# Kernel tuning notes

Measured on AMD Instinct MI355X. Metric: run time of the kernel, lower is better.

## Reference

```python
import jax, jax.numpy as jnp
import numpy as np
import math

B, C, D, H, W = 1, 64, 16, 16, 16
HEADS = 4
HD = C // HEADS  # head_dim = 16


def conv3d(x, w, b, pad):
    # x: [B,C,D,H,W], w: [O,I,kd,kh,kw], pad: (pd,ph,pw)
    y = jax.lax.conv_general_dilated(
        x, w, window_strides=(1, 1, 1),
        padding=[(p, p) for p in pad],
        dimension_numbers=('NCDHW', 'OIDHW', 'NCDHW'))
    return y + b[None, :, None, None, None]


def setup_inputs() -> dict:
    key = jax.random.key(0)
    ks = jax.random.split(key, 10)
    s = 0.02
    return {
        'x': jax.random.normal(ks[0], (B, C, D, H, W), jnp.float32),
        'gamma': jax.random.normal(ks[1], (1,), jnp.float32),
        'w_sp': jax.random.normal(ks[2], (C, C, 1, 3, 3), jnp.float32) * s,
        'b_sp': jax.random.normal(ks[3], (C,), jnp.float32) * s,
        'w_spec': jax.random.normal(ks[4], (C, C, 3, 1, 1), jnp.float32) * s,
        'b_spec': jax.random.normal(ks[5], (C,), jnp.float32) * s,
        'w_qkv': jax.random.normal(ks[6], (3 * C, C, 1, 1, 1), jnp.float32) * s,
        'b_qkv': jax.random.normal(ks[7], (3 * C,), jnp.float32) * s,
        'w_proj': jax.random.normal(ks[8], (C, C, 1, 1, 1), jnp.float32) * s,
        'b_proj': jax.random.normal(ks[9], (C,), jnp.float32) * s,
    }


def _decay_exponent(dtype):
    # Faithful to the torch permute quirk (requires H == W):
    # exponent[i,j,k,m,n,o] = |i-m| + |j-k| + |n-o|
    dd = jnp.abs(jnp.arange(D)[:, None] - jnp.arange(D)[None, :]).astype(dtype)  # [D,D]
    hh = jnp.abs(jnp.arange(H)[:, None] - jnp.arange(H)[None, :]).astype(dtype)  # [H,H]
    ww = jnp.abs(jnp.arange(W)[:, None] - jnp.arange(W)[None, :]).astype(dtype)  # [W,W]
    return (dd[:, None, None, :, None, None]      # i (axis0), m (axis3)
            + hh[None, :, :, None, None, None]    # j (axis1), k (axis2)
            + ww[None, None, None, None, :, :])   # n (axis4), o (axis5)


def _forward(x, gamma, w_sp, b_sp, w_spec, b_spec, w_qkv, b_qkv, w_proj, b_proj):
    x = conv3d(x, w_sp, b_sp, (0, 1, 1))
    x = conv3d(x, w_spec, b_spec, (1, 0, 0))
    qkv = conv3d(x, w_qkv, b_qkv, (0, 0, 0))
    q, k, v = jnp.split(qkv, 3, axis=1)
    rs = lambda t: t.reshape(B, HEADS, HD, D, H, W)
    q, k, v = rs(q), rs(k), rs(v)

    g = jax.nn.sigmoid(gamma[0])
    decay = g ** _decay_exponent(x.dtype)  # [D,H,W,D,W,W] (H==W)

    # attn[b,h,i,j,k,m,n,o]: (i,j,k)=query D,H,W ; (m,n,o)=key D,H,W
    attn = jnp.einsum('bhdijk,bhdmno->bhijkmno', q, k) / math.sqrt(HD)
    attn = jax.nn.softmax(attn * decay, axis=-1)  # softmax over key-W axis o only
    out = jnp.einsum('bhijkmno,bhdmno->bhdijk', attn, v)
    out = out.reshape(B, C, D, H, W)
    return conv3d(out, w_proj, b_proj, (0, 0, 0))


def reference(x, gamma, w_sp, b_sp, w_spec, b_spec, w_qkv, b_qkv, w_proj, b_proj):
    return _forward(x, gamma, w_sp, b_sp, w_spec, b_spec, w_qkv, b_qkv, w_proj, b_proj)
```

## Files before the change

### kernel.cpp

```cpp
#include <hip/hip_runtime.h>
#include <math.h>

#define CN   262144
#define BTP 196
#define PTP 68

typedef __attribute__((ext_vector_type(8))) short short8;
typedef __attribute__((ext_vector_type(4))) short short4v;
typedef __attribute__((ext_vector_type(4))) float float4v;

static __device__ __forceinline__ unsigned short f2bf(float f) {
    union { float f; unsigned u; } v; v.f = f;
    unsigned r = (v.u + 0x7FFFu + ((v.u >> 16) & 1u)) >> 16;
    return (unsigned short)r;
}

__global__ __launch_bounds__(512, 4) void conv_sp_wfuse_kernel(
        const float* __restrict__ x, const float* __restrict__ w,
        const float* __restrict__ b, float* __restrict__ y,
        const float* __restrict__ w_spec, const float* __restrict__ b_spec,
        const float* __restrict__ w_qkv, const float* __restrict__ b_qkv,
        unsigned short* __restrict__ wfb, float* __restrict__ bfv) {
    if (blockIdx.x >= 1024) {
        int idx = (blockIdx.x - 1024) * 512 + threadIdx.x;
        int oc = idx / 192;
        int r  = idx % 192;
        float s = 0.f;
        #pragma unroll 8
        for (int ci = 0; ci < 64; ++ci)
            s += w_qkv[oc * 64 + ci] * w_spec[ci * 192 + r];
        if (oc < 64) s *= 0.25f;
        wfb[oc * 192 + r] = f2bf(s);
        if (idx < 192) {
            float t = b_qkv[idx];
            for (int ci = 0; ci < 64; ++ci) t += w_qkv[idx * 64 + ci] * b_spec[ci];
            if (idx < 64) t *= 0.25f;
            bfv[idx] = t;
        }
        return;
    }
    __shared__ float ws[576];
    __shared__ float red[8][256];
    int co = blockIdx.x >> 4;
    int d  = blockIdx.x & 15;
    int tid = threadIdx.x;
    for (int idx = tid; idx < 576; idx += 512) ws[idx] = w[co * 576 + idx];
    __syncthreads();
    int og  = tid & 63;
    int grp = tid >> 6;
    int h = og >> 2, wq = og & 3;
    float ax = 0.f, ay = 0.f, az = 0.f, aw = 0.f;
    #pragma unroll 4
    for (int c2 = 0; c2 < 8; ++c2) {
        int ci = grp * 8 + c2;
        const float* row = x + ci * 4096 + d * 256;
        const float* wc  = ws + ci * 9;
        #pragma unroll
        for (int dh = 0; dh < 3; ++dh) {
            int hh = h + dh - 1;
            if (hh < 0 || hh > 15) continue;
            const float* r = row + hh * 16 + wq * 4;
            float4 q0 = *(const float4*)r;
            float lm = (wq > 0) ? r[-1] : 0.f;
            float rp = (wq < 3) ? r[4]  : 0.f;
            float wL = wc[dh * 3 + 0], wM = wc[dh * 3 + 1], wR = wc[dh * 3 + 2];
            ax += wL * lm   + wM * q0.x + wR * q0.y;
            ay += wL * q0.x + wM * q0.y + wR * q0.z;
            az += wL * q0.y + wM * q0.z + wR * q0.w;
            aw += wL * q0.z + wM * q0.w + wR * rp;
        }
    }
    float4 part = {ax, ay, az, aw};
    *(float4*)&red[grp][og * 4] = part;
    __syncthreads();
    if (tid < 256) {
        float s = b[co];
        #pragma unroll
        for (int g = 0; g < 8; ++g) s += red[g][tid];
        y[co * 4096 + d * 256 + tid] = s;
    }
}

__global__ __launch_bounds__(512, 4) void qkv_mfma_kernel(
        const float* __restrict__ y1, const unsigned short* __restrict__ wfb,
        const float* __restrict__ bfv,
        unsigned short* __restrict__ qb, unsigned short* __restrict__ kb,
        unsigned short* __restrict__ vtb) {
    __shared__ __align__(16) unsigned short Bt[32 * BTP];
    int bI  = blockIdx.x;
    int ocg = bI % 3;
    int pq  = (bI / 3) & 7;
    int d   = bI / 24;
    int tid = threadIdx.x;

    {
        int px  = tid & 31;
        int cig = tid >> 5;
        const float* yb = y1 + d * 256 + pq * 32 + px;
        #pragma unroll
        for (int cc = 0; cc < 4; ++cc) {
            int ci = cig * 4 + cc;
            const float* yc = yb + ci * 4096;
            #pragma unroll
            for (int t = 0; t < 3; ++t) {
                float v = 0.f;
                if (!((d == 0 && t == 0) || (d == 15 && t == 2)))
                    v = yc[(t - 1) * 256];
                Bt[px * BTP + ci * 3 + t] = f2bf(v);
            }
        }
    }

    int wv = tid >> 6, lane = tid & 63;
    int quad = lane >> 4, l15 = lane & 15;
    int Mt = wv >> 1;
    int nt = wv & 1;

    short8 af[6];
    {
        const unsigned short* ab = wfb + (ocg * 64 + Mt * 16 + l15) * 192 + quad * 8;
        #pragma unroll
        for (int ks = 0; ks < 6; ++ks) af[ks] = *(const short8*)(ab + ks * 32);
    }
    float bias[4];
    #pragma unroll
    for (int r = 0; r < 4; ++r) bias[r] = bfv[ocg * 64 + Mt * 16 + quad * 4 + r];

    __syncthreads();

    float4v czero = {0.f, 0.f, 0.f, 0.f};
    float4v acc = czero;
    {
        const unsigned short* brow = Bt + (nt * 16 + l15) * BTP + quad * 8;
        #pragma unroll
        for (int ks = 0; ks < 6; ++ks) {
            short4v lo = *(const short4v*)(brow + ks * 32);
            short4v hi = *(const short4v*)(brow + ks * 32 + 4);
            short8 bf8 = {lo[0], lo[1], lo[2], lo[3], hi[0], hi[1], hi[2], hi[3]};
            acc = __builtin_amdgcn_mfma_f32_16x16x32_bf16(af[ks], bf8, acc, 0, 0, 0);
        }
    }

    {
        int p = d * 256 + pq * 32 + nt * 16 + l15;
        if (ocg == 2) {
            int h = (p >> 4) & 15, w0 = p & 15;
            int kap = 8 * (w0 >> 2) + 4 * (h & 1) + (w0 & 3);
            unsigned short* dst = vtb + ((Mt * 16 + d) * 8 + (h >> 1)) * 512
                                      + (quad * 4) * 32 + kap;
            #pragma unroll
            for (int r = 0; r < 4; ++r) dst[r * 32] = f2bf(acc[r] + bias[r]);
        } else {
            unsigned short* dst = (ocg == 0 ? qb : kb) + Mt * 65536 + p * 16 + quad * 4;
            unsigned t0 = (unsigned)f2bf(acc[0] + bias[0])
                        | ((unsigned)f2bf(acc[1] + bias[1]) << 16);
            unsigned t1 = (unsigned)f2bf(acc[2] + bias[2])
                        | ((unsigned)f2bf(acc[3] + bias[3]) << 16);
            *(unsigned*)dst = t0;
            *(unsigned*)(dst + 2) = t1;
        }
    }
}

__global__ __launch_bounds__(512, 4) void attn_kernel(
        const unsigned short* __restrict__ qb, const unsigned short* __restrict__ kb,
        const unsigned short* __restrict__ vtb, const float* __restrict__ gamma,
        float* __restrict__ aoall) {
    __shared__ __align__(16) unsigned short ksh[2][4096];
    __shared__ __align__(16) unsigned short vsh[2][4096];
    __shared__ float gp[32];
    int tid = threadIdx.x;
    int bI = blockIdx.x;
    int head = bI >> 8;
    int mg   = (bI >> 5) & 7;
    int oct  = bI & 31;

    if (tid < 32) {
        float g = 1.f / (1.f + __expf(-gamma[0]));
        gp[tid] = __powf(g, (float)tid);
    }

    int wv = tid >> 6, lane = tid & 63;
    int quad = lane >> 4, l15 = lane & 15;
    int t = oct * 8 + wv;
    int i = t >> 4, j = t & 15;

    short8 zero8 = {0, 0, 0, 0, 0, 0, 0, 0};
    float4v czero = {0.f, 0.f, 0.f, 0.f};
    short8 qf = zero8;
    if (quad < 2)
        qf = *(const short8*)(qb + head * 65536 + (t * 16 + l15) * 16 + quad * 8);

    const unsigned short* kbh = kb  + head * 65536 + mg * 2 * 4096;
    const unsigned short* vbh = vtb + head * 65536 + mg * 2 * 4096;
    float4 k0 = ((const float4*)kbh)[tid];
    float4 v0 = ((const float4*)vbh)[tid];
    float4 k1 = ((const float4*)(kbh + 4096))[tid];
    float4 v1 = ((const float4*)(vbh + 4096))[tid];
    ((float4*)ksh[0])[tid] = k0;
    ((float4*)vsh[0])[tid] = v0;
    ((float4*)ksh[1])[tid] = k1;
    ((float4*)vsh[1])[tid] = v1;
    __syncthreads();

    float wd[4];
    #pragma unroll
    for (int r = 0; r < 4; ++r)
        wd[r] = gp[abs(l15 - (quad * 4 + r))] * 1.4426950408889634f;

    float4v O = czero;
    #pragma unroll
    for (int mm = 0; mm < 2; ++mm) {
        int m = mg * 2 + mm;
        const unsigned short* kk = ksh[mm];
        const unsigned short* vv = vsh[mm];
        int eim = abs(i - m);
        #pragma unroll
        for (int np = 0; np < 8; ++np) {
            union { unsigned u[4]; short8 s8; } a2u;
            #pragma unroll
            for (int s = 0; s < 2; ++s) {
                int n = np * 2 + s;
                short8 a1 = zero8;
                if (quad < 2)
                    a1 = *(const short8*)(kk + n * 256 + l15 * 16 + quad * 8);
                float4v d1 = __builtin_amdgcn_mfma_f32_16x16x32_bf16(a1, qf, czero, 0, 0, 0);
                float smn = gp[eim + abs(j - n)];
                float e0 = __builtin_amdgcn_exp2f(d1[0] * smn * wd[0]);
                float e1 = __builtin_amdgcn_exp2f(d1[1] * smn * wd[1]);
                float e2 = __builtin_amdgcn_exp2f(d1[2] * smn * wd[2]);
                float e3 = __builtin_amdgcn_exp2f(d1[3] * smn * wd[3]);
                float sm = e0 + e1 + e2 + e3;
                sm += __shfl_xor(sm, 16);
                sm += __shfl_xor(sm, 32);
                float inv = __builtin_amdgcn_rcpf(sm);
                union { float f; unsigned u; } p0, p1, p2, p3;
                p0.f = e0 * inv; p1.f = e1 * inv;
                p2.f = e2 * inv; p3.f = e3 * inv;
                a2u.u[s * 2]     = ((p0.u + 0x8000u) >> 16) | ((p1.u + 0x8000u) & 0xFFFF0000u);
                a2u.u[s * 2 + 1] = ((p2.u + 0x8000u) >> 16) | ((p3.u + 0x8000u) & 0xFFFF0000u);
            }
            short8 b2 = *(const short8*)(vv + np * 512 + l15 * 32 + quad * 8);
            O = __builtin_amdgcn_mfma_f32_16x16x32_bf16(a2u.s8, b2, O, 0, 0, 0);
        }
    }

    float* aop = aoall + mg * CN;
    float4 ov = {O[0], O[1], O[2], O[3]};
    *(float4*)(aop + (head * 16 + l15) * 4096 + t * 16 + quad * 4) = ov;
}

__global__ __launch_bounds__(256, 8) void proj_mfma_kernel(
        const float* __restrict__ aoall,
        const float* __restrict__ w, const float* __restrict__ b,
        float* __restrict__ out) {
    __shared__ __align__(16) unsigned short Bt[16 * PTP];
    int d   = blockIdx.x >> 4;
    int p16 = blockIdx.x & 15;
    int tid = threadIdx.x;

    {
        int px = tid & 15, cig = tid >> 4;
        int gbase = d * 256 + p16 * 16 + px;
        #pragma unroll
        for (int cc = 0; cc < 4; ++cc) {
            int ci = cig * 4 + cc;
            int ga = ci * 4096 + gbase;
            float v = 0.f;
            #pragma unroll
            for (int k = 0; k < 8; ++k) v += aoall[k * CN + ga];
            Bt[px * PTP + ci] = f2bf(v);
        }
    }
    __syncthreads();

    int wv = tid >> 6, lane = tid & 63;
    int quad = lane >> 4, l15 = lane & 15;
    float4v czero = {0.f, 0.f, 0.f, 0.f};
    float4v acc = czero;

    short8 af[2];
    const float* wsrc = w + (wv * 16 + l15) * 64 + quad * 8;
    #pragma unroll
    for (int ks = 0; ks < 2; ++ks) {
        float4 wa = *(const float4*)(wsrc + ks * 32);
        float4 wb = *(const float4*)(wsrc + ks * 32 + 4);
        short8 a8 = {(short)f2bf(wa.x), (short)f2bf(wa.y), (short)f2bf(wa.z),
                     (short)f2bf(wa.w), (short)f2bf(wb.x), (short)f2bf(wb.y),
                     (short)f2bf(wb.z), (short)f2bf(wb.w)};
        af[ks] = a8;
    }
    const unsigned short* brow = Bt + l15 * PTP + quad * 8;
    #pragma unroll
    for (int ks = 0; ks < 2; ++ks) {
        short4v lo = *(const short4v*)(brow + ks * 32);
        short4v hi = *(const short4v*)(brow + ks * 32 + 4);
        short8 bf8 = {lo[0], lo[1], lo[2], lo[3], hi[0], hi[1], hi[2], hi[3]};
        acc = __builtin_amdgcn_mfma_f32_16x16x32_bf16(af[ks], bf8, acc, 0, 0, 0);
    }

    int p = d * 256 + p16 * 16 + l15;
    #pragma unroll
    for (int r = 0; r < 4; ++r) {
        int oc = wv * 16 + quad * 4 + r;
        out[oc * 4096 + p] = acc[r] + b[oc];
    }
}

extern "C" void kernel_launch(void* const* d_in, const int* in_sizes, int n_in,
                              void* d_out, int out_size, void* d_ws, size_t ws_size,
                              hipStream_t stream) {
    const float* x      = (const float*)d_in[0];
    const float* gamma  = (const float*)d_in[1];
    const float* w_sp   = (const float*)d_in[2];
    const float* b_sp   = (const float*)d_in[3];
    const float* w_spec = (const float*)d_in[4];
    const float* b_spec = (const float*)d_in[5];
    const float* w_qkv  = (const float*)d_in[6];
    const float* b_qkv  = (const float*)d_in[7];
    const float* w_proj = (const float*)d_in[8];
    const float* b_proj = (const float*)d_in[9];
    float* out = (float*)d_out;

    float* ws = (float*)d_ws;
    float* y1  = ws;
    unsigned short* wfb = (unsigned short*)(ws + CN);
    float* bfv = ws + CN + 20480;
    unsigned short* qb  = (unsigned short*)(ws + 2 * CN);
    unsigned short* kb  = (unsigned short*)(ws + 2 * CN + CN / 2);
    unsigned short* vtb = (unsigned short*)(ws + 3 * CN);
    float* aoall = ws + 3 * CN + CN / 2;

    conv_sp_wfuse_kernel<<<1096, 512, 0, stream>>>(x, w_sp, b_sp, y1,
                                                   w_spec, b_spec, w_qkv, b_qkv,
                                                   wfb, bfv);
    qkv_mfma_kernel <<< 384, 512, 0, stream>>>(y1, wfb, bfv, qb, kb, vtb);
    attn_kernel     <<<1024, 512, 0, stream>>>(qb, kb, vtb, gamma, aoall);
    proj_mfma_kernel<<< 256, 256, 0, stream>>>(aoall, w_proj, b_proj, out);
}
```

Baseline: 134.6 us.

## Move spatial 3x3 conv onto bf16 MFMA with a separate weight-prep kernel

Rewrites the spatial 1x3x3 convolution from scalar FP32 FMAs into an implicit GEMM on bf16 16x16x32 MFMA. Input patches are staged through LDS one kernel row at a time, and the next row is prefetched into registers while the current one is multiplied. A new weight-prep kernel converts w_sp to a bf16 layout and absorbs the fused qkv weight precompute that used to run in the extra conv blocks. This adds one kernel launch and lowers the conv's precision to bf16.

Measured after the change: 118.0 us (median of 2 runs). -12.4%, faster.

```diff
diff --git a/kernel.cpp b/kernel.cpp
--- a/kernel.cpp
+++ b/kernel.cpp
@@ -15,70 +15,108 @@
     return (unsigned short)r;
 }
 
-__global__ __launch_bounds__(512, 4) void conv_sp_wfuse_kernel(
-        const float* __restrict__ x, const float* __restrict__ w,
-        const float* __restrict__ b, float* __restrict__ y,
+__global__ __launch_bounds__(512) void wprep_kernel(
+        const float* __restrict__ w_sp,
         const float* __restrict__ w_spec, const float* __restrict__ b_spec,
         const float* __restrict__ w_qkv, const float* __restrict__ b_qkv,
+        unsigned short* __restrict__ wsb,
         unsigned short* __restrict__ wfb, float* __restrict__ bfv) {
-    if (blockIdx.x >= 1024) {
-        int idx = (blockIdx.x - 1024) * 512 + threadIdx.x;
-        int oc = idx / 192;
-        int r  = idx % 192;
+    int idx = blockIdx.x * 512 + threadIdx.x;
+    if (idx < 36864) {
+        int dh  = idx / 12288;
+        int rem = idx % 12288;
+        int co  = rem / 192;
+        int kp  = rem % 192;
+        int ci = kp / 3, dw = kp % 3;
+        wsb[idx] = f2bf(w_sp[co * 576 + ci * 9 + dh * 3 + dw]);
+    } else {
+        int j = idx - 36864;
+        int oc = j / 192;
+        int r  = j % 192;
         float s = 0.f;
         #pragma unroll 8
         for (int ci = 0; ci < 64; ++ci)
             s += w_qkv[oc * 64 + ci] * w_spec[ci * 192 + r];
         if (oc < 64) s *= 0.25f;
         wfb[oc * 192 + r] = f2bf(s);
-        if (idx < 192) {
-            float t = b_qkv[idx];
-            for (int ci = 0; ci < 64; ++ci) t += w_qkv[idx * 64 + ci] * b_spec[ci];
-            if (idx < 64) t *= 0.25f;
-            bfv[idx] = t;
-        }
-        return;
-    }
-    __shared__ float ws[576];
-    __shared__ float red[8][256];
-    int co = blockIdx.x >> 4;
-    int d  = blockIdx.x & 15;
+        if (j < 192) {
+            float t = b_qkv[j];
+            for (int ci = 0; ci < 64; ++ci) t += w_qkv[j * 64 + ci] * b_spec[ci];
+            if (j < 64) t *= 0.25f;
+            bfv[j] = t;
+        }
+    }
+}
+
+__global__ __launch_bounds__(256, 4) void conv_sp_mfma_kernel(
+        const float* __restrict__ x, const unsigned short* __restrict__ wsb,
+        const float* __restrict__ b_sp, float* __restrict__ y1) {
+    __shared__ __align__(16) unsigned short Bt[16 * BTP];
+    int d = blockIdx.x >> 4;
+    int h = blockIdx.x & 15;
     int tid = threadIdx.x;
-    for (int idx = tid; idx < 576; idx += 512) ws[idx] = w[co * 576 + idx];
-    __syncthreads();
-    int og  = tid & 63;
-    int grp = tid >> 6;
-    int h = og >> 2, wq = og & 3;
-    float ax = 0.f, ay = 0.f, az = 0.f, aw = 0.f;
-    #pragma unroll 4
-    for (int c2 = 0; c2 < 8; ++c2) {
-        int ci = grp * 8 + c2;
-        const float* row = x + ci * 4096 + d * 256;
-        const float* wc  = ws + ci * 9;
-        #pragma unroll
-        for (int dh = 0; dh < 3; ++dh) {
-            int hh = h + dh - 1;
-            if (hh < 0 || hh > 15) continue;
-            const float* r = row + hh * 16 + wq * 4;
-            float4 q0 = *(const float4*)r;
-            float lm = (wq > 0) ? r[-1] : 0.f;
-            float rp = (wq < 3) ? r[4]  : 0.f;
-            float wL = wc[dh * 3 + 0], wM = wc[dh * 3 + 1], wR = wc[dh * 3 + 2];
-            ax += wL * lm   + wM * q0.x + wR * q0.y;
-            ay += wL * q0.x + wM * q0.y + wR * q0.z;
-            az += wL * q0.y + wM * q0.z + wR * q0.w;
-            aw += wL * q0.z + wM * q0.w + wR * rp;
-        }
-    }
-    float4 part = {ax, ay, az, aw};
-    *(float4*)&red[grp][og * 4] = part;
-    __syncthreads();
-    if (tid < 256) {
-        float s = b[co];
-        #pragma unroll
-        for (int g = 0; g < 8; ++g) s += red[g][tid];
-        y[co * 4096 + d * 256 + tid] = s;
-    }
+    int px = tid & 15, cig = tid >> 4;
+
+    float rcur[12], rnxt[12];
+    #define LOAD_CHUNK(dh_, rr)                                            \
+        {                                                                  \
+            int hh = h + (dh_) - 1;                                        \
+            _Pragma("unroll")                                              \
+            for (int cc = 0; cc < 4; ++cc) {                               \
+                int ci = cig * 4 + cc;                                     \
+                const float* xr = x + ci * 4096 + d * 256 + hh * 16;       \
+                _Pragma("unroll")                                          \
+                for (int dw = 0; dw < 3; ++dw) {                           \
+                    int ww = px + dw - 1;                                  \
+                    float v = 0.f;                                         \
+                    if (hh >= 0 && hh <= 15 && ww >= 0 && ww <= 15)        \
+                        v = xr[ww];                                        \
+                    (rr)[cc * 3 + dw] = v;                                 \
+                }                                                          \
+            }                                                              \
+        }
+
+    LOAD_CHUNK(0, rcur);
+
+    int wv = tid >> 6, lane = tid & 63;
+    int quad = lane >> 4, l15 = lane & 15;
+    float4v czero = {0.f, 0.f, 0.f, 0.f};
+    float4v acc = czero;
+
+    #pragma unroll
+    for (int c = 0; c < 3; ++c) {
+        __syncthreads();
+        #pragma unroll
+        for (int cc = 0; cc < 4; ++cc) {
+            int ci = cig * 4 + cc;
+            Bt[px * BTP + ci * 3 + 0] = f2bf(rcur[cc * 3 + 0]);
+            Bt[px * BTP + ci * 3 + 1] = f2bf(rcur[cc * 3 + 1]);
+            Bt[px * BTP + ci * 3 + 2] = f2bf(rcur[cc * 3 + 2]);
+        }
+        __syncthreads();
+        if (c < 2) LOAD_CHUNK(c + 1, rnxt);
+
+        const unsigned short* ab = wsb + c * 12288 + (wv * 16 + l15) * 192 + quad * 8;
+        const unsigned short* brow = Bt + l15 * BTP + quad * 8;
+        #pragma unroll
+        for (int ks = 0; ks < 6; ++ks) {
+            short8 af = *(const short8*)(ab + ks * 32);
+            short4v lo = *(const short4v*)(brow + ks * 32);
+            short4v hi = *(const short4v*)(brow + ks * 32 + 4);
+            short8 bf8 = {lo[0], lo[1], lo[2], lo[3], hi[0], hi[1], hi[2], hi[3]};
+            acc = __builtin_amdgcn_mfma_f32_16x16x32_bf16(af, bf8, acc, 0, 0, 0);
+        }
+        #pragma unroll
+        for (int q2 = 0; q2 < 12; ++q2) rcur[q2] = rnxt[q2];
+    }
+
+    int p = d * 256 + h * 16 + l15;
+    #pragma unroll
+    for (int r = 0; r < 4; ++r) {
+        int co = wv * 16 + quad * 4 + r;
+        y1[co * 4096 + p] = acc[r] + b_sp[co];
+    }
+    #undef LOAD_CHUNK
 }
 
 __global__ __launch_bounds__(512, 4) void qkv_mfma_kernel(
@@ -326,15 +364,16 @@
     float* y1  = ws;
     unsigned short* wfb = (unsigned short*)(ws + CN);
     float* bfv = ws + CN + 20480;
+    unsigned short* wsb = (unsigned short*)(ws + CN + 24576);
     unsigned short* qb  = (unsigned short*)(ws + 2 * CN);
     unsigned short* kb  = (unsigned short*)(ws + 2 * CN + CN / 2);
     unsigned short* vtb = (unsigned short*)(ws + 3 * CN);
     float* aoall = ws + 3 * CN + CN / 2;
 
-    conv_sp_wfuse_kernel<<<1096, 512, 0, stream>>>(x, w_sp, b_sp, y1,
-                                                   w_spec, b_spec, w_qkv, b_qkv,
-                                                   wfb, bfv);
-    qkv_mfma_kernel <<< 384, 512, 0, stream>>>(y1, wfb, bfv, qb, kb, vtb);
-    attn_kernel     <<<1024, 512, 0, stream>>>(qb, kb, vtb, gamma, aoall);
-    proj_mfma_kernel<<< 256, 256, 0, stream>>>(aoall, w_proj, b_proj, out);
-}
+    wprep_kernel       <<< 144, 512, 0, stream>>>(w_sp, w_spec, b_spec,
+                                                  w_qkv, b_qkv, wsb, wfb, bfv);
+    conv_sp_mfma_kernel<<< 256, 256, 0, stream>>>(x, wsb, b_sp, y1);
+    qkv_mfma_kernel    <<< 384, 512, 0, stream>>>(y1, wfb, bfv, qb, kb, vtb);
+    attn_kernel        <<<1024, 512, 0, stream>>>(qb, kb, vtb, gamma, aoall);
+    proj_mfma_kernel   <<< 256, 256, 0, stream>>>(aoall, w_proj, b_proj, out);
+}
```
